# Kernel optimization log

Hardware: AMD Instinct MI355X
Metric: run time of the kernel (lower is better)

Reference implementation:

```python
import jax, jax.numpy as jnp
import numpy as np

N = 100000          # nodes
E = 1200000         # edges
IN_DIM = 128
HID = 64
NUM_CLASSES = 5
NUM_GRAPHS = 128


def setup_inputs() -> dict:
    key = jax.random.key(0)
    ks = jax.random.split(key, 12)
    x = jax.random.normal(ks[0], (N, IN_DIM), dtype=jnp.float32)
    edge_index = jax.random.randint(ks[1], (2, E), 0, N, dtype=jnp.int64)
    batch = jnp.sort(jax.random.randint(ks[2], (N,), 0, NUM_GRAPHS, dtype=jnp.int64))
    def glorot(k, shape):
        lim = np.sqrt(6.0 / (shape[0] + shape[1]))
        return jax.random.uniform(k, shape, jnp.float32, -lim, lim)
    W1 = glorot(ks[3], (IN_DIM, HID)); b1 = jnp.zeros((HID,), jnp.float32)
    W2 = glorot(ks[4], (HID, HID));    b2 = jnp.zeros((HID,), jnp.float32)
    W3 = glorot(ks[5], (HID, HID));    b3 = jnp.zeros((HID,), jnp.float32)
    Wc = glorot(ks[6], (HID, NUM_CLASSES)); bc = jnp.zeros((NUM_CLASSES,), jnp.float32)
    return {"x": x, "edge_index": edge_index, "batch": batch,
            "W1": W1, "b1": b1, "W2": W2, "b2": b2, "W3": W3, "b3": b3,
            "Wc": Wc, "bc": bc}


def _gcn_norm(edge_index, n_nodes):
    # PyG GCNConv: add self-loops, symmetric normalization D^-1/2 (A+I) D^-1/2
    loop = jnp.arange(n_nodes, dtype=edge_index.dtype)
    src = jnp.concatenate([edge_index[0], loop])  # [E+N]
    dst = jnp.concatenate([edge_index[1], loop])
    deg = jax.ops.segment_sum(jnp.ones_like(dst, dtype=jnp.float32), dst,
                              num_segments=n_nodes)
    dinv = jnp.where(deg > 0, jax.lax.rsqrt(deg), 0.0)
    norm = dinv[src] * dinv[dst]                   # [E+N]
    return src, dst, norm


def _gcn_conv(x, src, dst, norm, W, b, n_nodes):
    h = x @ W                                      # [N, out]
    msg = h[src] * norm[:, None]                   # gather + scale
    agg = jax.ops.segment_sum(msg, dst, num_segments=n_nodes)  # scatter-add
    return agg + b


def reference(x, edge_index, batch, W1, b1, W2, b2, W3, b3, Wc, bc):
    src, dst, norm = _gcn_norm(edge_index, N)
    h = jax.nn.relu(_gcn_conv(x, src, dst, norm, W1, b1, N))
    h = jax.nn.relu(_gcn_conv(h, src, dst, norm, W2, b2, N))
    h = jax.nn.relu(_gcn_conv(h, src, dst, norm, W3, b3, N))
    # global_mean_pool over batch ids
    sums = jax.ops.segment_sum(h, batch, num_segments=NUM_GRAPHS)
    counts = jax.ops.segment_sum(jnp.ones((N,), jnp.float32), batch,
                                 num_segments=NUM_GRAPHS)
    pooled = sums / jnp.maximum(counts, 1.0)[:, None]  # [G, HID]
    return pooled @ Wc + bc                             # [G, num_classes]
```

## Files before the change

kernel.cpp:

```cpp
#include <hip/hip_runtime.h>
#include <hip/hip_bf16.h>

#define NN 100000
#define NE 1200000
#define IND 128
#define HID 64
#define NC 5
#define NG 128
#define NB 391
#define GB 1172
#define G1 3125

typedef float v2f __attribute__((ext_vector_type(2)));

static __device__ __forceinline__ float bf2f(unsigned short u) {
    union { unsigned int i; float f; } x;
    x.i = (unsigned int)u << 16;
    return x.f;
}
static __device__ __forceinline__ unsigned short f2bf(float f) {
    union { float f; unsigned int i; } x;
    x.f = f;
    unsigned int r = (x.i + 0x7fffu + ((x.i >> 16) & 1u)) >> 16;
    return (unsigned short)r;
}
static __device__ __forceinline__ unsigned short f2fp8x2(float a, float b) {
    int p = __builtin_amdgcn_cvt_pk_fp8_f32(a, b, 0, false);
    return (unsigned short)(p & 0xffff);
}
static __device__ __forceinline__ void fp8acc(unsigned int u, float& a0, float& a1, float& a2, float& a3) {
    v2f lo = __builtin_amdgcn_cvt_pk_f32_fp8(u, false);
    v2f hi = __builtin_amdgcn_cvt_pk_f32_fp8(u, true);
    a0 += lo.x; a1 += lo.y; a2 += hi.x; a3 += hi.y;
}

__global__ __launch_bounds__(256) void k_hist(const int* __restrict__ dst, int* __restrict__ cnt,
                                              int* __restrict__ rank) {
    int e = blockIdx.x * 256 + threadIdx.x;
    if (e < NE) rank[e] = atomicAdd(&cnt[dst[e]], 1);
}

__global__ __launch_bounds__(256) void k_scan1(const int* __restrict__ cnt, int* __restrict__ exc,
                                               int* __restrict__ bsum, float* __restrict__ dinv) {
    __shared__ int lds[256];
    int tid = threadIdx.x;
    int i = blockIdx.x * 256 + tid;
    int v = (i < NN) ? cnt[i] : 0;
    lds[tid] = v;
    __syncthreads();
    for (int off = 1; off < 256; off <<= 1) {
        int t = (tid >= off) ? lds[tid - off] : 0;
        __syncthreads();
        lds[tid] += t;
        __syncthreads();
    }
    if (i < NN) {
        exc[i] = lds[tid] - v;
        dinv[i] = rsqrtf((float)v + 1.0f);
    }
    if (tid == 255) bsum[blockIdx.x] = lds[255];
}

__global__ __launch_bounds__(256) void k_scan23(const int* __restrict__ exc, const int* __restrict__ bsum,
                                                int* __restrict__ row_ptr) {
    __shared__ int lds[256];
    int tid = threadIdx.x;
    int me = blockIdx.x;
    int v = 0;
    if (tid < me) v = bsum[tid];
    if (tid + 256 < me) v += bsum[tid + 256];
    lds[tid] = v;
    __syncthreads();
    for (int off = 128; off > 0; off >>= 1) {
        if (tid < off) lds[tid] += lds[tid + off];
        __syncthreads();
    }
    int base = lds[0];
    int i = me * 256 + tid;
    if (i < NN) row_ptr[i] = exc[i] + base;
    if (i == 0) row_ptr[NN] = NE;
}

__global__ __launch_bounds__(256) void k_fused1(
    const float* __restrict__ X, const float* __restrict__ W,
    const float* __restrict__ dinv, unsigned short* __restrict__ out_f8,
    const int* __restrict__ src, const int* __restrict__ dst,
    const int* __restrict__ row_ptr, const int* __restrict__ rank,
    int* __restrict__ src_sorted,
    const int* __restrict__ batch, int* __restrict__ start)
{
    __shared__ float lds[IND * HID + 32 * IND];
    int tid = threadIdx.x;

    if (blockIdx.x < GB) {
        int t = blockIdx.x * 256 + tid;
        const int T = GB * 256;
#pragma unroll
        for (int u = 0; u < 4; ++u) {
            int e = t + u * T;
            if (e < NE) src_sorted[row_ptr[dst[e]] + rank[e]] = src[e];
        }
        return;
    }
    if (blockIdx.x >= GB + G1) {
        int i = (blockIdx.x - GB - G1) * 256 + tid;
        if (i >= NN) return;
        int b = batch[i];
        if (i == 0) {
            for (int g = 0; g <= b; ++g) start[g] = 0;
        } else {
            int p = batch[i - 1];
            for (int g = p + 1; g <= b; ++g) start[g] = i;
        }
        if (i == NN - 1) {
            for (int g = b + 1; g <= NG; ++g) start[g] = NN;
        }
        return;
    }

    float* Wl = lds;
    float* xl = lds + IND * HID;
    int n0 = (blockIdx.x - GB) * 32;
    int c = tid & 31;
    int s = tid >> 5;

    {
        const float4* Wg = (const float4*)W;
        float4* Wl4 = (float4*)Wl;
#pragma unroll
        for (int i = 0; i < IND * 16 / 256; ++i) Wl4[i * 256 + tid] = Wg[i * 256 + tid];
    }
    {
        const float4* Xg = (const float4*)X;
        float4* xl4 = (float4*)xl;
        const float4 z = {0.f, 0.f, 0.f, 0.f};
#pragma unroll
        for (int i = 0; i < 32 * IND / 4 / 256; ++i) {
            int idx = i * 256 + tid;
            int node = n0 + idx / (IND / 4);
            xl4[idx] = (node < NN) ? Xg[(size_t)n0 * (IND / 4) + idx] : z;
        }
    }
    __syncthreads();

    float acc[4][2];
#pragma unroll
    for (int r = 0; r < 4; ++r) { acc[r][0] = 0.f; acc[r][1] = 0.f; }

#pragma unroll 4
    for (int k0 = 0; k0 < IND; k0 += 4) {
        float4 xv[4];
#pragma unroll
        for (int r = 0; r < 4; ++r) xv[r] = *(const float4*)&xl[(s * 4 + r) * IND + k0];
#pragma unroll
        for (int kk = 0; kk < 4; ++kk) {
            float w0 = Wl[(k0 + kk) * HID + 2 * c];
            float w1 = Wl[(k0 + kk) * HID + 2 * c + 1];
#pragma unroll
            for (int r = 0; r < 4; ++r) {
                float xe = (kk == 0) ? xv[r].x : (kk == 1) ? xv[r].y : (kk == 2) ? xv[r].z : xv[r].w;
                acc[r][0] = fmaf(xe, w0, acc[r][0]);
                acc[r][1] = fmaf(xe, w1, acc[r][1]);
            }
        }
    }

#pragma unroll
    for (int r = 0; r < 4; ++r) {
        int n = n0 + s * 4 + r;
        if (n < NN) {
            float dn = dinv[n];
            out_f8[(size_t)n * 32 + c] = f2fp8x2(acc[r][0] * dn, acc[r][1] * dn);
        }
    }
}

__global__ __launch_bounds__(256) void k_aggregate(const unsigned int* __restrict__ hW8,
                                                   const int* __restrict__ srcs,
                                                   const int* __restrict__ row_ptr,
                                                   const float* __restrict__ dinv,
                                                   const float* __restrict__ b,
                                                   unsigned int* __restrict__ outb) {
    int tid = threadIdx.x;
    int lane = tid & 63;
    int grp = lane >> 4;
    int li = lane & 15;
    int n = blockIdx.x * 4 + (tid >> 6);

    float a0 = 0.f, a1 = 0.f, a2 = 0.f, a3 = 0.f;
    if (grp == 0) {
        unsigned int su = hW8[(size_t)n * 16 + li];
        fp8acc(su, a0, a1, a2, a3);
    }

    int e = row_ptr[n];
    int end = row_ptr[n + 1];

    for (; e + 7 < end; e += 8) {
        int sA = srcs[e + grp];
        int sB = srcs[e + 4 + grp];
        unsigned int uA = hW8[(size_t)sA * 16 + li];
        unsigned int uB = hW8[(size_t)sB * 16 + li];
        fp8acc(uA, a0, a1, a2, a3);
        fp8acc(uB, a0, a1, a2, a3);
    }
    if (e + 3 < end) {
        int sA = srcs[e + grp];
        unsigned int uA = hW8[(size_t)sA * 16 + li];
        fp8acc(uA, a0, a1, a2, a3);
        e += 4;
    }
    int rem = end - e;
    if (grp < rem) {
        int sA = srcs[e + grp];
        unsigned int uA = hW8[(size_t)sA * 16 + li];
        fp8acc(uA, a0, a1, a2, a3);
    }

    a0 += __shfl_xor(a0, 16, 64);
    a1 += __shfl_xor(a1, 16, 64);
    a2 += __shfl_xor(a2, 16, 64);
    a3 += __shfl_xor(a3, 16, 64);
    a0 += __shfl_xor(a0, 32, 64);
    a1 += __shfl_xor(a1, 32, 64);
    a2 += __shfl_xor(a2, 32, 64);
    a3 += __shfl_xor(a3, 32, 64);

    if (lane < 16) {
        float dn = dinv[n];
        float4 bv = ((const float4*)b)[li];
        float v0 = fmaxf(fmaf(dn, a0, bv.x), 0.0f);
        float v1 = fmaxf(fmaf(dn, a1, bv.y), 0.0f);
        float v2 = fmaxf(fmaf(dn, a2, bv.z), 0.0f);
        float v3 = fmaxf(fmaf(dn, a3, bv.w), 0.0f);
        uint2 p;
        p.x = (unsigned int)f2bf(v0) | ((unsigned int)f2bf(v1) << 16);
        p.y = (unsigned int)f2bf(v2) | ((unsigned int)f2bf(v3) << 16);
        ((uint2*)outb)[(size_t)n * 16 + li] = p;
    }
}

__global__ __launch_bounds__(256) void k_gemm_bf(const unsigned short* __restrict__ X,
                                                 const float* __restrict__ W,
                                                 const float* __restrict__ dinv,
                                                 unsigned short* __restrict__ out_f8) {
    __shared__ float Wl[HID * HID];
    __shared__ float xl[64 * HID];
    int tid = threadIdx.x;
    int n0 = blockIdx.x * 64;

    {
        const float4* Wg = (const float4*)W;
        float4* Wl4 = (float4*)Wl;
#pragma unroll
        for (int i = 0; i < HID * HID / 4 / 256; ++i) Wl4[i * 256 + tid] = Wg[i * 256 + tid];
    }
    {
        const uint4* Xg = (const uint4*)X;
#pragma unroll
        for (int i = 0; i < 2; ++i) {
            int idx = i * 256 + tid;
            int ln = idx >> 3;
            int k0 = (idx & 7) * 8;
            int node = n0 + ln;
            float f[8];
            if (node < NN) {
                uint4 u = Xg[(size_t)n0 * 8 + idx];
                f[0] = bf2f((unsigned short)(u.x & 0xffff));
                f[1] = bf2f((unsigned short)(u.x >> 16));
                f[2] = bf2f((unsigned short)(u.y & 0xffff));
                f[3] = bf2f((unsigned short)(u.y >> 16));
                f[4] = bf2f((unsigned short)(u.z & 0xffff));
                f[5] = bf2f((unsigned short)(u.z >> 16));
                f[6] = bf2f((unsigned short)(u.w & 0xffff));
                f[7] = bf2f((unsigned short)(u.w >> 16));
            } else {
#pragma unroll
                for (int q = 0; q < 8; ++q) f[q] = 0.f;
            }
#pragma unroll
            for (int q = 0; q < 8; ++q) xl[ln * HID + k0 + q] = f[q];
        }
    }
    __syncthreads();

    int c = tid & 31;
    int s = tid >> 5;
    float acc[8][2];
#pragma unroll
    for (int r = 0; r < 8; ++r) { acc[r][0] = 0.f; acc[r][1] = 0.f; }

#pragma unroll 4
    for (int k0 = 0; k0 < HID; k0 += 4) {
        float4 xv[8];
#pragma unroll
        for (int r = 0; r < 8; ++r) xv[r] = *(const float4*)&xl[(s * 8 + r) * HID + k0];
#pragma unroll
        for (int kk = 0; kk < 4; ++kk) {
            float w0 = Wl[(k0 + kk) * HID + 2 * c];
            float w1 = Wl[(k0 + kk) * HID + 2 * c + 1];
#pragma unroll
            for (int r = 0; r < 8; ++r) {
                float xe = (kk == 0) ? xv[r].x : (kk == 1) ? xv[r].y : (kk == 2) ? xv[r].z : xv[r].w;
                acc[r][0] = fmaf(xe, w0, acc[r][0]);
                acc[r][1] = fmaf(xe, w1, acc[r][1]);
            }
        }
    }

#pragma unroll
    for (int r = 0; r < 8; ++r) {
        int n = n0 + s * 8 + r;
        if (n < NN) {
            float dn = dinv[n];
            out_f8[(size_t)n * 32 + c] = f2fp8x2(acc[r][0] * dn, acc[r][1] * dn);
        }
    }
}

__global__ __launch_bounds__(256) void k_pool_head(const unsigned short* __restrict__ h,
                                                   const int* __restrict__ start,
                                                   const float* __restrict__ Wc, const float* __restrict__ bc,
                                                   float* __restrict__ out) {
    __shared__ float part[4][HID];
    int g = blockIdx.x;
    int tid = threadIdx.x;
    int j = tid & 63, w = tid >> 6;
    int beg = start[g], end = start[g + 1];
    float acc = 0.0f;
    for (int n = beg + w; n < end; n += 4) acc += bf2f(h[n * HID + j]);
    part[w][j] = acc;
    __syncthreads();
    if (w == 0) {
        float s = part[0][j] + part[1][j] + part[2][j] + part[3][j];
        float cnt = (float)(end - beg);
        float p = s / fmaxf(cnt, 1.0f);
#pragma unroll
        for (int c = 0; c < NC; ++c) {
            float v = p * Wc[j * NC + c];
            for (int off = 32; off > 0; off >>= 1) v += __shfl_down(v, off);
            if (j == 0) out[g * NC + c] = v + bc[c];
        }
    }
}

extern "C" void kernel_launch(void* const* d_in, const int* in_sizes, int n_in,
                              void* d_out, int out_size, void* d_ws, size_t ws_size,
                              hipStream_t stream) {
    const float* x  = (const float*)d_in[0];
    const int* ei   = (const int*)d_in[1];
    const int* bat  = (const int*)d_in[2];
    const float* W1 = (const float*)d_in[3];
    const float* b1 = (const float*)d_in[4];
    const float* W2 = (const float*)d_in[5];
    const float* b2 = (const float*)d_in[6];
    const float* W3 = (const float*)d_in[7];
    const float* b3 = (const float*)d_in[8];
    const float* Wc = (const float*)d_in[9];
    const float* bc = (const float*)d_in[10];
    float* out = (float*)d_out;

    const int* src = ei;
    const int* dst = ei + NE;

    char* wsb = (char*)d_ws;
    float* dinv         = (float*)wsb;
    int*   row_ptr      = (int*)(wsb + 400000);
    int*   srcs         = (int*)(wsb + 800016);
    unsigned short* hF8 = (unsigned short*)(wsb + 5600016);
    unsigned short* hBF = (unsigned short*)(wsb + 18400016);
    int*   cnt          = (int*)(wsb + 31200016);
    int*   exc          = (int*)(wsb + 31600016);
    int*   bsum         = (int*)(wsb + 32000016);
    int*   rank         = (int*)(wsb + 32002064);
    int*   start        = (int*)(wsb + 36802064);

    const int gE = (NE + 255) / 256;

    hipMemsetAsync(cnt, 0, NN * sizeof(int), stream);
    k_hist<<<gE, 256, 0, stream>>>(dst, cnt, rank);
    k_scan1<<<NB, 256, 0, stream>>>(cnt, exc, bsum, dinv);
    k_scan23<<<NB, 256, 0, stream>>>(exc, bsum, row_ptr);

    k_fused1<<<GB + G1 + NB, 256, 0, stream>>>(x, W1, dinv, hF8, src, dst, row_ptr, rank, srcs, bat, start);

    k_aggregate<<<NN / 4, 256, 0, stream>>>((const unsigned int*)hF8, srcs, row_ptr, dinv, b1, (unsigned int*)hBF);
    k_gemm_bf<<<(NN + 63) / 64, 256, 0, stream>>>(hBF, W2, dinv, hF8);
    k_aggregate<<<NN / 4, 256, 0, stream>>>((const unsigned int*)hF8, srcs, row_ptr, dinv, b2, (unsigned int*)hBF);
    k_gemm_bf<<<(NN + 63) / 64, 256, 0, stream>>>(hBF, W3, dinv, hF8);
    k_aggregate<<<NN / 4, 256, 0, stream>>>((const unsigned int*)hF8, srcs, row_ptr, dinv, b3, (unsigned int*)hBF);

    k_pool_head<<<NG, 256, 0, stream>>>(hBF, start, Wc, bc, out);
}
```

Measured before the change: 343.6 us.

## Split fp8 feature table into two column planes and aggregate each plane separately

```diff
diff --git a/kernel.cpp b/kernel.cpp
--- a/kernel.cpp
+++ b/kernel.cpp
@@ -165,12 +165,14 @@
         }
     }
 
+    int P = c >> 4;
+    int slot = c & 15;
 #pragma unroll
     for (int r = 0; r < 4; ++r) {
         int n = n0 + s * 4 + r;
         if (n < NN) {
             float dn = dinv[n];
-            out_f8[(size_t)n * 32 + c] = f2fp8x2(acc[r][0] * dn, acc[r][1] * dn);
+            out_f8[(size_t)P * NN * 16 + (size_t)n * 16 + slot] = f2fp8x2(acc[r][0] * dn, acc[r][1] * dn);
         }
     }
 }
@@ -180,43 +182,49 @@
                                                    const int* __restrict__ row_ptr,
                                                    const float* __restrict__ dinv,
                                                    const float* __restrict__ b,
-                                                   unsigned int* __restrict__ outb) {
+                                                   unsigned int* __restrict__ outb,
+                                                   int P) {
+    const unsigned int* __restrict__ plane = hW8 + (size_t)P * NN * 8;
     int tid = threadIdx.x;
     int lane = tid & 63;
-    int grp = lane >> 4;
-    int li = lane & 15;
+    int grp = lane >> 3;
+    int li = lane & 7;
     int n = blockIdx.x * 4 + (tid >> 6);
 
     float a0 = 0.f, a1 = 0.f, a2 = 0.f, a3 = 0.f;
     if (grp == 0) {
-        unsigned int su = hW8[(size_t)n * 16 + li];
+        unsigned int su = plane[(size_t)n * 8 + li];
         fp8acc(su, a0, a1, a2, a3);
     }
 
     int e = row_ptr[n];
     int end = row_ptr[n + 1];
 
-    for (; e + 7 < end; e += 8) {
+    for (; e + 15 < end; e += 16) {
         int sA = srcs[e + grp];
-        int sB = srcs[e + 4 + grp];
-        unsigned int uA = hW8[(size_t)sA * 16 + li];
-        unsigned int uB = hW8[(size_t)sB * 16 + li];
+        int sB = srcs[e + 8 + grp];
+        unsigned int uA = plane[(size_t)sA * 8 + li];
+        unsigned int uB = plane[(size_t)sB * 8 + li];
         fp8acc(uA, a0, a1, a2, a3);
         fp8acc(uB, a0, a1, a2, a3);
     }
-    if (e + 3 < end) {
+    if (e + 7 < end) {
         int sA = srcs[e + grp];
-        unsigned int uA = hW8[(size_t)sA * 16 + li];
+        unsigned int uA = plane[(size_t)sA * 8 + li];
         fp8acc(uA, a0, a1, a2, a3);
-        e += 4;
+        e += 8;
     }
     int rem = end - e;
     if (grp < rem) {
         int sA = srcs[e + grp];
-        unsigned int uA = hW8[(size_t)sA * 16 + li];
+        unsigned int uA = plane[(size_t)sA * 8 + li];
         fp8acc(uA, a0, a1, a2, a3);
     }
 
+    a0 += __shfl_xor(a0, 8, 64);
+    a1 += __shfl_xor(a1, 8, 64);
+    a2 += __shfl_xor(a2, 8, 64);
+    a3 += __shfl_xor(a3, 8, 64);
     a0 += __shfl_xor(a0, 16, 64);
     a1 += __shfl_xor(a1, 16, 64);
     a2 += __shfl_xor(a2, 16, 64);
@@ -226,9 +234,9 @@
     a2 += __shfl_xor(a2, 32, 64);
     a3 += __shfl_xor(a3, 32, 64);
 
-    if (lane < 16) {
+    if (lane < 8) {
         float dn = dinv[n];
-        float4 bv = ((const float4*)b)[li];
+        float4 bv = ((const float4*)b)[8 * P + li];
         float v0 = fmaxf(fmaf(dn, a0, bv.x), 0.0f);
         float v1 = fmaxf(fmaf(dn, a1, bv.y), 0.0f);
         float v2 = fmaxf(fmaf(dn, a2, bv.z), 0.0f);
@@ -236,7 +244,7 @@
         uint2 p;
         p.x = (unsigned int)f2bf(v0) | ((unsigned int)f2bf(v1) << 16);
         p.y = (unsigned int)f2bf(v2) | ((unsigned int)f2bf(v3) << 16);
-        ((uint2*)outb)[(size_t)n * 16 + li] = p;
+        ((uint2*)outb)[(size_t)n * 16 + 8 * P + li] = p;
     }
 }
 
@@ -308,12 +316,14 @@
         }
     }
 
+    int P = c >> 4;
+    int slot = c & 15;
 #pragma unroll
     for (int r = 0; r < 8; ++r) {
         int n = n0 + s * 8 + r;
         if (n < NN) {
             float dn = dinv[n];
-            out_f8[(size_t)n * 32 + c] = f2fp8x2(acc[r][0] * dn, acc[r][1] * dn);
+            out_f8[(size_t)P * NN * 16 + (size_t)n * 16 + slot] = f2fp8x2(acc[r][0] * dn, acc[r][1] * dn);
         }
     }
 }
@@ -384,11 +394,14 @@
 
     k_fused1<<<GB + G1 + NB, 256, 0, stream>>>(x, W1, dinv, hF8, src, dst, row_ptr, rank, srcs, bat, start);
 
-    k_aggregate<<<NN / 4, 256, 0, stream>>>((const unsigned int*)hF8, srcs, row_ptr, dinv, b1, (unsigned int*)hBF);
+    k_aggregate<<<NN / 4, 256, 0, stream>>>((const unsigned int*)hF8, srcs, row_ptr, dinv, b1, (unsigned int*)hBF, 0);
+    k_aggregate<<<NN / 4, 256, 0, stream>>>((const unsigned int*)hF8, srcs, row_ptr, dinv, b1, (unsigned int*)hBF, 1);
     k_gemm_bf<<<(NN + 63) / 64, 256, 0, stream>>>(hBF, W2, dinv, hF8);
-    k_aggregate<<<NN / 4, 256, 0, stream>>>((const unsigned int*)hF8, srcs, row_ptr, dinv, b2, (unsigned int*)hBF);
+    k_aggregate<<<NN / 4, 256, 0, stream>>>((const unsigned int*)hF8, srcs, row_ptr, dinv, b2, (unsigned int*)hBF, 0);
+    k_aggregate<<<NN / 4, 256, 0, stream>>>((const unsigned int*)hF8, srcs, row_ptr, dinv, b2, (unsigned int*)hBF, 1);
     k_gemm_bf<<<(NN + 63) / 64, 256, 0, stream>>>(hBF, W3, dinv, hF8);
-    k_aggregate<<<NN / 4, 256, 0, stream>>>((const unsigned int*)hF8, srcs, row_ptr, dinv, b3, (unsigned int*)hBF);
+    k_aggregate<<<NN / 4, 256, 0, stream>>>((const unsigned int*)hF8, srcs, row_ptr, dinv, b3, (unsigned int*)hBF, 0);
+    k_aggregate<<<NN / 4, 256, 0, stream>>>((const unsigned int*)hF8, srcs, row_ptr, dinv, b3, (unsigned int*)hBF, 1);
 
     k_pool_head<<<NG, 256, 0, stream>>>(hBF, start, Wc, bc, out);
 }
```

After: 424.4 us. 23.5% more time.
